# Kernel tuning notes

Hardware: AMD Instinct MI355X
Metric: run time of the kernel (lower is better)

Reference implementation:

```python
import math
import jax, jax.numpy as jnp
import numpy as np

EPS = 1e-5
RATIO = 0.5


def gcn_conv(x, src, dst, ew, W, b):
    # GCNConv(add_self_loops=True, normalize=True, improved=True): self-loop fill = 2.0
    N = x.shape[0]
    h = x @ W  # [N, Cout]
    deg = jax.ops.segment_sum(ew, dst, num_segments=N) + 2.0
    dinv = jnp.where(deg > 0, deg ** -0.5, 0.0)
    norm = dinv[src] * ew * dinv[dst]  # [E]
    agg = jax.ops.segment_sum(h[src] * norm[:, None], dst, num_segments=N)
    return agg + (2.0 * dinv * dinv)[:, None] * h + b


def batch_norm(x, g, b):
    # training-mode BatchNorm1d over nodes (biased variance)
    mu = x.mean(0)
    var = x.var(0)
    return (x - mu) * jax.lax.rsqrt(var + EPS) * g + b


def topk_pool(x, src, dst, ew, p):
    # TopKPooling: score = tanh(x.p/||p||), keep top ceil(ratio*N), x' = x[perm]*score[perm]
    N = x.shape[0]
    k = int(math.ceil(RATIO * N))
    score = jnp.tanh((x @ p) / jnp.linalg.norm(p))
    vals, perm = jax.lax.top_k(score, k)
    xk = x[perm] * vals[:, None]
    new_idx = jnp.full((N,), -1, jnp.int32).at[perm].set(jnp.arange(k, dtype=jnp.int32))
    ns, nd = new_idx[src], new_idx[dst]
    keep = (ns >= 0) & (nd >= 0)
    # keep fixed edge count; dropped edges get weight 0 -> contribute nothing
    return xk, jnp.where(keep, ns, 0), jnp.where(keep, nd, 0), jnp.where(keep, ew, 0.0), perm


def encode(x, src, dst, ew, mW, mb, g1, b1, cW, cb, g2, b2):
    x = batch_norm(jax.nn.relu(x @ mW + mb), g1, b1)  # MLP: Lin -> ReLU -> BN
    x = gcn_conv(x, src, dst, ew, cW, cb)
    return jax.nn.relu(batch_norm(x, g2, b2))


def unet(x, edge_src, edge_dst,
         e0_mlp_W, e0_mlp_b, e0_bn1_g, e0_bn1_b, e0_conv_W, e0_conv_b, e0_n_g, e0_n_b,
         e1_p, e1_mlp_W, e1_mlp_b, e1_bn1_g, e1_bn1_b, e1_conv_W, e1_conv_b, e1_n_g, e1_n_b,
         e2_p, e2_mlp_W, e2_mlp_b, e2_bn1_g, e2_bn1_b, e2_conv_W, e2_conv_b, e2_n_g, e2_n_b,
         d2_W, d2_b, d1_W, d1_b, d0_W, d0_b):
    E = edge_src.shape[0]
    ew0 = jnp.ones((E,), x.dtype)
    # encoder0 (no pool)
    x1 = encode(x, edge_src, edge_dst, ew0, e0_mlp_W, e0_mlp_b, e0_bn1_g, e0_bn1_b,
                e0_conv_W, e0_conv_b, e0_n_g, e0_n_b)
    # encoder1 (pool 0.5)
    xp, s1, t1, ew1, perm1 = topk_pool(x1, edge_src, edge_dst, ew0, e1_p)
    x2 = encode(xp, s1, t1, ew1, e1_mlp_W, e1_mlp_b, e1_bn1_g, e1_bn1_b,
                e1_conv_W, e1_conv_b, e1_n_g, e1_n_b)
    # encoder2 (pool 0.5)
    xp, s2, t2, ew2, perm2 = topk_pool(x2, s1, t1, ew1, e2_p)
    x3 = encode(xp, s2, t2, ew2, e2_mlp_W, e2_mlp_b, e2_bn1_g, e2_bn1_b,
                e2_conv_W, e2_conv_b, e2_n_g, e2_n_b)
    # decoder2 + unpool into x2 via perm2: up[perm]=(x+res[perm])/2, up[~perm]=res
    d = jax.nn.relu(gcn_conv(x3, s2, t2, ew2, d2_W, d2_b))
    xu = x2.at[perm2].set((d + x2[perm2]) * 0.5)
    # decoder1 + unpool into x1 via perm1
    d = jax.nn.relu(gcn_conv(xu, s1, t1, ew1, d1_W, d1_b))
    xu = x1.at[perm1].set((d + x1[perm1]) * 0.5)
    # decoder0 on the original graph, no activation
    return gcn_conv(xu, edge_src, edge_dst, ew0, d0_W, d0_b)


def setup_inputs() -> dict:
    key = jax.random.key(0)
    N, E, C = 100000, 1600000, [16, 64, 128, 256]
    ks = iter(jax.random.split(key, 64))
    nk = lambda: next(ks)

    def glorot(shape):
        s = math.sqrt(6.0 / (shape[0] + shape[1]))
        return jax.random.uniform(nk(), shape, minval=-s, maxval=s, dtype=jnp.float32)

    inp = {
        'x': jax.random.normal(nk(), (N, C[0]), jnp.float32),
        'edge_src': jax.random.randint(nk(), (E,), 0, N, jnp.int32),
        'edge_dst': jax.random.randint(nk(), (E,), 0, N, jnp.int32),
    }
    for i, (ci, co) in enumerate(zip(C[:-1], C[1:])):
        pre = f'e{i}_'
        if i > 0:
            inp[pre + 'p'] = jax.random.normal(nk(), (ci,), jnp.float32)
        inp[pre + 'mlp_W'] = glorot((ci, co)); inp[pre + 'mlp_b'] = jnp.zeros((co,), jnp.float32)
        inp[pre + 'bn1_g'] = jnp.ones((co,), jnp.float32); inp[pre + 'bn1_b'] = jnp.zeros((co,), jnp.float32)
        inp[pre + 'conv_W'] = glorot((co, co)); inp[pre + 'conv_b'] = jnp.zeros((co,), jnp.float32)
        inp[pre + 'n_g'] = jnp.ones((co,), jnp.float32); inp[pre + 'n_b'] = jnp.zeros((co,), jnp.float32)
    inp['d2_W'] = glorot((256, 128)); inp['d2_b'] = jnp.zeros((128,), jnp.float32)
    inp['d1_W'] = glorot((128, 64)); inp['d1_b'] = jnp.zeros((64,), jnp.float32)
    inp['d0_W'] = glorot((64, 16)); inp['d0_b'] = jnp.zeros((16,), jnp.float32)
    return inp


def reference(x, edge_src, edge_dst,
              e0_mlp_W, e0_mlp_b, e0_bn1_g, e0_bn1_b, e0_conv_W, e0_conv_b, e0_n_g, e0_n_b,
              e1_p, e1_mlp_W, e1_mlp_b, e1_bn1_g, e1_bn1_b, e1_conv_W, e1_conv_b, e1_n_g, e1_n_b,
              e2_p, e2_mlp_W, e2_mlp_b, e2_bn1_g, e2_bn1_b, e2_conv_W, e2_conv_b, e2_n_g, e2_n_b,
              d2_W, d2_b, d1_W, d1_b, d0_W, d0_b):
    return unet(x, edge_src, edge_dst,
                e0_mlp_W, e0_mlp_b, e0_bn1_g, e0_bn1_b, e0_conv_W, e0_conv_b, e0_n_g, e0_n_b,
                e1_p, e1_mlp_W, e1_mlp_b, e1_bn1_g, e1_bn1_b, e1_conv_W, e1_conv_b, e1_n_g, e1_n_b,
                e2_p, e2_mlp_W, e2_mlp_b, e2_bn1_g, e2_bn1_b, e2_conv_W, e2_conv_b, e2_n_g, e2_n_b,
                d2_W, d2_b, d1_W, d1_b, d0_W, d0_b)
```

## Files before the change

### kernel.cpp

```cpp
#include <hip/hip_runtime.h>
#include <math.h>

static inline int cdiv(int a, int b){ return (a + b - 1) / b; }

#define SCAN_CHUNK 4096
#define BCHUNK 4096

typedef _Float16 v4h __attribute__((ext_vector_type(4)));
typedef float    v4f __attribute__((ext_vector_type(4)));
typedef _Float16 h2  __attribute__((ext_vector_type(2)));


__global__ void k_count0(const int* __restrict__ dst, int* __restrict__ cnt, int E){
  int i = blockIdx.x*blockDim.x + threadIdx.x;
  if (i < E) atomicAdd(&cnt[dst[i]], 1);
}

__global__ __launch_bounds__(256) void k_bucket(const int* __restrict__ src, const int* __restrict__ dst,
                        int E, int* __restrict__ gcur, unsigned int* __restrict__ bout){
  __shared__ int lcnt[256], gbase[256];
  int t = threadIdx.x;
  lcnt[t] = 0;
  __syncthreads();
  int base = blockIdx.x*BCHUNK;
  int end = min(base + BCHUNK, E);
  for (int i = base + t; i < end; i += 256) atomicAdd(&lcnt[dst[i] >> 9], 1);
  __syncthreads();
  gbase[t] = lcnt[t] ? atomicAdd(&gcur[t], lcnt[t]) : 0;
  __syncthreads();
  lcnt[t] = 0;
  __syncthreads();
  for (int i = base + t; i < end; i += 256){
    int s = src[i], d = dst[i];
    int b = d >> 9;
    int pos = gbase[b] + atomicAdd(&lcnt[b], 1);
    bout[pos] = ((unsigned int)s << 9) | (unsigned int)(d & 511);
  }
}

__global__ __launch_bounds__(256) void k_fill_b(const unsigned int* __restrict__ bout,
                        const int* __restrict__ rowptr, int* __restrict__ fillg,
                        int* __restrict__ cols, int N, int BPB){
  int b = blockIdx.x / BPB, sub = blockIdx.x % BPB;
  int r0 = b << 9;
  int r1 = min(r0 + 512, N);
  int start = rowptr[r0], end = rowptr[r1];
  for (int i = start + sub*256 + threadIdx.x; i < end; i += BPB*256){
    unsigned int v = bout[i];
    int d = r0 + (int)(v & 511u);
    int pos = rowptr[d] + atomicAdd(&fillg[d], 1);
    cols[pos] = (int)(v >> 9);
  }
}


__global__ __launch_bounds__(256) void k_csr_keep(const int* __restrict__ rowptrA, const int* __restrict__ colsA,
                         const int* __restrict__ nidx, int* __restrict__ tmp,
                         int* __restrict__ cnt, int NA){
  int t = threadIdx.x;
  int g = (blockIdx.x*256 + t) >> 4;
  int lane = t & 15;
  if (g >= NA) return;
  int m = nidx[g];
  if (m < 0) return;
  int jb = rowptrA[g], je = rowptrA[g+1];
  int run = 0;
  int shift = (t & 63) & ~15;
  for (int j0 = jb; j0 < je; j0 += 16){
    int j = j0 + lane;
    int s = -1;
    if (j < je) s = nidx[colsA[j]];
    bool keep = s >= 0;
    unsigned long long bal = __ballot(keep);
    unsigned int gm = (unsigned int)(bal >> shift) & 0xFFFFu;
    if (keep) tmp[jb + run + __popc(gm & ((1u << lane) - 1))] = s;
    run += __popc(gm);
  }
  if (lane == 0) cnt[m] = run;
}

__global__ __launch_bounds__(256) void k_csr_copy(const int* __restrict__ rowptrA, const int* __restrict__ nidx,
                         const int* __restrict__ tmp, const int* __restrict__ rowptrB,
                         int* __restrict__ colsB, int NA){
  int t = threadIdx.x;
  int g = (blockIdx.x*256 + t) >> 4;
  int lane = t & 15;
  if (g >= NA) return;
  int m = nidx[g];
  if (m < 0) return;
  int jbA = rowptrA[g];
  int db = rowptrB[m], n = rowptrB[m+1] - db;
  for (int j = lane; j < n; j += 16) colsB[db + j] = tmp[jbA + j];
}


__global__ __launch_bounds__(256) void k_scan_p1(const int* __restrict__ in, int nIn, int* __restrict__ bsum){
  __shared__ int sh[256];
  int base = blockIdx.x*SCAN_CHUNK;
  int end = min(base + SCAN_CHUNK, nIn);
  int s = 0;
  for (int i = base + threadIdx.x; i < end; i += 256) s += in[i];
  sh[threadIdx.x] = s; __syncthreads();
  for (int o = 128; o > 0; o >>= 1){
    if (threadIdx.x < o) sh[threadIdx.x] += sh[threadIdx.x + o];
    __syncthreads();
  }
  if (threadIdx.x == 0) bsum[blockIdx.x] = sh[0];
}

__global__ __launch_bounds__(256) void k_scan_p2(int* __restrict__ bsum, int nb){
  __shared__ int sh[256];
  int t = threadIdx.x;
  int v = (t < nb) ? bsum[t] : 0;
  sh[t] = v; __syncthreads();
  for (int o = 1; o < 256; o <<= 1){
    int u = (t >= o) ? sh[t-o] : 0;
    __syncthreads();
    sh[t] += u;
    __syncthreads();
  }
  if (t < nb) bsum[t] = sh[t] - v;
}

__global__ __launch_bounds__(256) void k_scan_p3(const int* __restrict__ cnt, const int* __restrict__ bsum,
                        int* __restrict__ rowptr, float* __restrict__ dinv,
                        int* __restrict__ gcur, int nIn){
  int t = threadIdx.x;
  int tb = blockIdx.x*SCAN_CHUNK + t*16;
  int my[16]; int s = 0;
#pragma unroll
  for (int j = 0; j < 16; ++j){
    int i = tb + j;
    int v = (i < nIn) ? cnt[i] : 0;
    my[j] = v; s += v;
  }
  __shared__ int sh[256];
  sh[t] = s; __syncthreads();
  for (int o = 1; o < 256; o <<= 1){
    int u = (t >= o) ? sh[t-o] : 0;
    __syncthreads();
    sh[t] += u;
    __syncthreads();
  }
  int run = bsum[blockIdx.x] + sh[t] - s;
#pragma unroll
  for (int j = 0; j < 16; ++j){
    int i = tb + j;
    if (i < nIn){
      rowptr[i] = run;
      if (dinv) dinv[i] = rsqrtf((float)my[j] + 2.0f);
      if (gcur && (i & 511) == 0) gcur[i >> 9] = run;
      run += my[j];
    } else if (i == nIn){
      rowptr[nIn] = run;
    }
  }
}


__global__ void k_prep_w_el(const float* __restrict__ W, const float* __restrict__ ss,
                            _Float16* __restrict__ Whi, _Float16* __restrict__ Wlo,
                            float* __restrict__ bias2, const float* __restrict__ bias,
                            int KM, int M, int mshift, int mmask){
  int idx = blockIdx.x*256 + threadIdx.x;
  if (idx >= KM) return;
  int k = idx >> mshift, m = idx & mmask;
  float w = W[idx];
  if (ss) w *= ss[k];
  _Float16 hi = (_Float16)w;
  size_t oidx = ((size_t)(k >> 2)*M + m)*4 + (k & 3);
  Whi[oidx] = hi;
  if (Wlo) Wlo[oidx] = (_Float16)(w - (float)hi);
  if (k == 0) bias2[m] = bias ? bias[m] : 0.f;
}

__global__ void k_prep_bias(const float* __restrict__ W, const float* __restrict__ ss,
                            float* __restrict__ bias2, int K, int M){
  int m = blockIdx.x;
  int lane = threadIdx.x;
  float s = 0.f;
  for (int k = lane; k < K; k += 64) s = fmaf(ss[K + k], W[(size_t)k*M + m], s);
  for (int o = 32; o > 0; o >>= 1) s += __shfl_down(s, o, 64);
  if (lane == 0) bias2[m] = s;
}


template<int SPLIT>
__global__ __launch_bounds__(256) void k_gemm16(
    const float* __restrict__ A, const _Float16* __restrict__ Whi,
    const _Float16* __restrict__ Wlo, const float* __restrict__ bias2,
    float* __restrict__ Out32, _Float16* __restrict__ Out16,
    float* __restrict__ stats, const int* __restrict__ permA,
    const float* __restrict__ valA, int N, int K, int M, int relu)
{
  __shared__ float sacc[64], s2acc[64];
  int tid = threadIdx.x;
  if (stats){
    if (tid < 64){ sacc[tid] = 0.f; s2acc[tid] = 0.f; }
    __syncthreads();
  }
  int wave = tid >> 6, lane = tid & 63;
  int g = lane >> 4, r = lane & 15;
  int wrow0 = blockIdx.x*256 + wave*64;
  int col0 = blockIdx.y*64;
  int nf = (M - col0) >> 4; if (nf > 4) nf = 4;

  int srow[4]; float sclr[4];
#pragma unroll
  for (int rt = 0; rt < 4; ++rt){
    int arow = wrow0 + rt*16 + r;
    if (arow < N){
      int sr = permA ? permA[arow] : arow;
      srow[rt] = sr;
      sclr[rt] = permA ? valA[sr] : 1.f;
    } else { srow[rt] = -1; sclr[rt] = 0.f; }
  }

  v4f acc[4][4];
#pragma unroll
  for (int rt = 0; rt < 4; ++rt)
#pragma unroll
    for (int c = 0; c < 4; ++c) acc[rt][c] = (v4f){0.f,0.f,0.f,0.f};

  for (int k0 = 0; k0 < K; k0 += 16){
    int kb = (k0 >> 2) + g;
    v4h bh[4], bl[4];
#pragma unroll
    for (int c = 0; c < 4; ++c){
      if (c >= nf) continue;
      size_t bidx = ((size_t)kb*M + col0 + c*16 + r)*4;
      bh[c] = *(const v4h*)&Whi[bidx];
      if (SPLIT) bl[c] = *(const v4h*)&Wlo[bidx];
    }
    v4h ah[4], al[4];
#pragma unroll
    for (int rt = 0; rt < 4; ++rt){
      if (srow[rt] >= 0){
        float4 av = *(const float4*)&A[(size_t)srow[rt]*K + k0 + g*4];
        float xs[4] = {av.x*sclr[rt], av.y*sclr[rt], av.z*sclr[rt], av.w*sclr[rt]};
#pragma unroll
        for (int j = 0; j < 4; ++j){
          _Float16 hi = (_Float16)xs[j];
          ah[rt][j] = hi;
          if (SPLIT) al[rt][j] = (_Float16)(xs[j] - (float)hi);
        }
      } else {
#pragma unroll
        for (int j = 0; j < 4; ++j){ ah[rt][j] = (_Float16)0.f; if (SPLIT) al[rt][j] = (_Float16)0.f; }
      }
    }
#pragma unroll
    for (int rt = 0; rt < 4; ++rt){
#pragma unroll
      for (int c = 0; c < 4; ++c){
        if (c >= nf) continue;
        acc[rt][c] = __builtin_amdgcn_mfma_f32_16x16x16f16(ah[rt], bh[c], acc[rt][c], 0, 0, 0);
        if (SPLIT){
          acc[rt][c] = __builtin_amdgcn_mfma_f32_16x16x16f16(al[rt], bh[c], acc[rt][c], 0, 0, 0);
          acc[rt][c] = __builtin_amdgcn_mfma_f32_16x16x16f16(ah[rt], bl[c], acc[rt][c], 0, 0, 0);
        }
      }
    }
  }

#pragma unroll
  for (int c = 0; c < 4; ++c){
    if (c >= nf) continue;
    int col = col0 + c*16 + r;
    float bsv = bias2[col];
    float s = 0.f, s2 = 0.f;
#pragma unroll
    for (int rt = 0; rt < 4; ++rt){
#pragma unroll
      for (int i = 0; i < 4; ++i){
        int rr = wrow0 + rt*16 + g*4 + i;
        float v = acc[rt][c][i] + bsv;
        if (relu) v = fmaxf(v, 0.f);
        if (rr < N){
          if (Out32) Out32[(size_t)rr*M + col] = v;
          if (Out16) Out16[(size_t)rr*M + col] = (_Float16)v;
          s += v; s2 = fmaf(v, v, s2);
        }
      }
    }
    if (stats){
      s  += __shfl_xor(s, 16);  s  += __shfl_xor(s, 32);
      s2 += __shfl_xor(s2, 16); s2 += __shfl_xor(s2, 32);
      if (g == 0){
        atomicAdd(&sacc[c*16 + r], s);
        atomicAdd(&s2acc[c*16 + r], s2);
      }
    }
  }
  if (stats){
    __syncthreads();
    if (tid < 64 && col0 + tid < M){
      atomicAdd(&stats[col0 + tid], sacc[tid]);
      atomicAdd(&stats[M + col0 + tid], s2acc[tid]);
    }
  }
}


__global__ void k_bn_stats(const float* __restrict__ X, float* __restrict__ acc, int N, int C){
  int col = threadIdx.x % C;
  int rg  = threadIdx.x / C;
  int R   = blockDim.x / C;
  float s = 0.f, s2 = 0.f;
  for (int r = blockIdx.x*R + rg; r < N; r += gridDim.x*R){
    float v = X[(size_t)r*C + col];
    s += v; s2 += v*v;
  }
  __shared__ float sh[256], sh2[256];
  sh[threadIdx.x] = s; sh2[threadIdx.x] = s2;
  __syncthreads();
  if (rg == 0){
    for (int r = 1; r < R; ++r){ s += sh[r*C + col]; s2 += sh2[r*C + col]; }
    atomicAdd(&acc[col], s);
    atomicAdd(&acc[C + col], s2);
  }
}

__global__ void k_bn_final(const float* __restrict__ acc, const float* __restrict__ g,
                           const float* __restrict__ b, float* __restrict__ ss, int N, int C){
  int c = threadIdx.x;
  if (c >= C) return;
  float mu  = acc[c] / (float)N;
  float var = acc[C + c] / (float)N - mu*mu;
  float sc  = rsqrtf(var + 1e-5f) * g[c];
  ss[c]     = sc;
  ss[C + c] = b[c] - mu*sc;
}

__global__ void k_bn_apply(const float* __restrict__ X, float* __restrict__ Y,
                           const float* __restrict__ ss, int total, int C, int relu){
  int i = blockIdx.x*blockDim.x + threadIdx.x;
  if (i >= total) return;
  int c = i % C;
  float v = X[i]*ss[c] + ss[C + c];
  if (relu) v = fmaxf(v, 0.f);
  Y[i] = v;
}

__global__ void k_bnap_score(const float* __restrict__ X, float* __restrict__ Y,
                             const float* __restrict__ ss, const float* __restrict__ p,
                             float* __restrict__ val, unsigned int* __restrict__ key,
                             int N, int C){
  int wid  = (blockIdx.x*blockDim.x + threadIdx.x) >> 6;
  int lane = threadIdx.x & 63;
  if (wid >= N) return;
  float s = 0.f, np = 0.f;
  for (int c = lane; c < C; c += 64){
    float v = X[(size_t)wid*C + c]*ss[c] + ss[C + c];
    v = fmaxf(v, 0.f);
    Y[(size_t)wid*C + c] = v;
    float pv = p[c];
    s = fmaf(v, pv, s);
    np = fmaf(pv, pv, np);
  }
  for (int o = 32; o > 0; o >>= 1){ s += __shfl_down(s, o, 64); np += __shfl_down(np, o, 64); }
  if (lane == 0){
    float sc = tanhf(s * rsqrtf(np));
    val[wid] = sc;
    unsigned int b = __float_as_uint(sc);
    key[wid] = (b & 0x80000000u) ? ~b : (b | 0x80000000u);
  }
}


__device__ inline float2 ldpair(const float* h, size_t off){
  return *(const float2*)(h + off);
}
__device__ inline float2 ldpair(const _Float16* h, size_t off){
  h2 v = *(const h2*)(h + off);
  return make_float2((float)v[0], (float)v[1]);
}

template<int C, typename T>
__global__ void k_agg(const T* __restrict__ h, const int* __restrict__ rowptr,
                      const int* __restrict__ cols, const float* __restrict__ dinv,
                      const float* __restrict__ bias, float* __restrict__ out,
                      int N, int relu)
{
  constexpr int PAIRS = C/2;
  constexpr int TPN = (PAIRS < 64) ? PAIRS : 64;
  constexpr int R = PAIRS / TPN;
  int gid  = blockIdx.x*blockDim.x + threadIdx.x;
  int node = gid / TPN;
  int lane = gid % TPN;
  if (node >= N) return;
  float di = dinv[node];
  float2 acc[R];
#pragma unroll
  for (int r = 0; r < R; ++r) acc[r] = make_float2(0.f, 0.f);
  int j  = rowptr[node];
  int je = rowptr[node+1];
  for (; j + 4 <= je; j += 4){
    int s0 = cols[j], s1 = cols[j+1], s2 = cols[j+2], s3 = cols[j+3];
    float w0 = dinv[s0]*di, w1 = dinv[s1]*di, w2 = dinv[s2]*di, w3 = dinv[s3]*di;
#pragma unroll
    for (int r = 0; r < R; ++r){
      size_t po = (size_t)(lane + r*TPN)*2;
      float2 h0 = ldpair(h, (size_t)s0*C + po);
      float2 h1 = ldpair(h, (size_t)s1*C + po);
      float2 h2v = ldpair(h, (size_t)s2*C + po);
      float2 h3 = ldpair(h, (size_t)s3*C + po);
      acc[r].x = fmaf(w0, h0.x, acc[r].x); acc[r].y = fmaf(w0, h0.y, acc[r].y);
      acc[r].x = fmaf(w1, h1.x, acc[r].x); acc[r].y = fmaf(w1, h1.y, acc[r].y);
      acc[r].x = fmaf(w2, h2v.x, acc[r].x); acc[r].y = fmaf(w2, h2v.y, acc[r].y);
      acc[r].x = fmaf(w3, h3.x, acc[r].x); acc[r].y = fmaf(w3, h3.y, acc[r].y);
    }
  }
  for (; j < je; ++j){
    int s = cols[j];
    float wgt = dinv[s]*di;
#pragma unroll
    for (int r = 0; r < R; ++r){
      float2 hv = ldpair(h, (size_t)s*C + (size_t)(lane + r*TPN)*2);
      acc[r].x = fmaf(wgt, hv.x, acc[r].x);
      acc[r].y = fmaf(wgt, hv.y, acc[r].y);
    }
  }
  float sw = 2.f*di*di;
#pragma unroll
  for (int r = 0; r < R; ++r){
    int pc = (lane + r*TPN)*2;
    float2 hv = ldpair(h, (size_t)node*C + pc);
    float2 v;
    v.x = acc[r].x + sw*hv.x + bias[pc];
    v.y = acc[r].y + sw*hv.y + bias[pc+1];
    if (relu){ v.x = fmaxf(v.x, 0.f); v.y = fmaxf(v.y, 0.f); }
    *(float2*)&out[(size_t)node*C + pc] = v;
  }
}

template<typename T>
static void launch_agg(const T* h, const int* rp, const int* cl, const float* dv,
                       const float* bias, float* o, int N, int C, int relu, hipStream_t stream){
  int tpn = (C/2 < 64) ? C/2 : 64;
  dim3 g(cdiv(N*tpn, 256));
  switch (C){
    case 16:  k_agg<16,T> <<<g, dim3(256), 0, stream>>>(h, rp, cl, dv, bias, o, N, relu); break;
    case 64:  k_agg<64,T> <<<g, dim3(256), 0, stream>>>(h, rp, cl, dv, bias, o, N, relu); break;
    case 128: k_agg<128,T><<<g, dim3(256), 0, stream>>>(h, rp, cl, dv, bias, o, N, relu); break;
    case 256: k_agg<256,T><<<g, dim3(256), 0, stream>>>(h, rp, cl, dv, bias, o, N, relu); break;
  }
}


__global__ void k_hist_hi(const unsigned int* __restrict__ key, int N, unsigned int* __restrict__ hist){
  int i = blockIdx.x*blockDim.x + threadIdx.x;
  if (i < N) atomicAdd(&hist[key[i] >> 16], 1u);
}

__global__ void k_hist_lo(const unsigned int* __restrict__ key, int N,
                          const int* __restrict__ state, unsigned int* __restrict__ hist){
  int i = blockIdx.x*blockDim.x + threadIdx.x;
  if (i >= N) return;
  unsigned int kk = key[i];
  if ((int)(kk >> 16) == state[1]) atomicAdd(&hist[kk & 0xffffu], 1u);
}

__global__ void k_scan_hist(unsigned int* __restrict__ hist, int* __restrict__ state,
                            int karg, int kidx, int bidx, int ridx){
  __shared__ unsigned int part[1024];
  __shared__ unsigned int suff[1024];
  int t = threadIdx.x;
  unsigned int s = 0;
  int base = t*64;
  for (int j = 0; j < 64; ++j) s += hist[base + j];
  part[t] = s;
  suff[t] = s;
  __syncthreads();
  for (int o = 1; o < 1024; o <<= 1){
    unsigned int v = (t + o < 1024) ? suff[t + o] : 0u;
    __syncthreads();
    suff[t] += v;
    __syncthreads();
  }
  unsigned int k = (unsigned int)((kidx >= 0) ? state[kidx] : karg);
  unsigned int above = suff[t] - part[t];
  if (above < k && above + part[t] >= k){
    unsigned int cum = above;
    for (int b = 63; b >= 0; --b){
      unsigned int c = hist[base + b];
      if (cum + c >= k){ state[bidx] = base + b; state[ridx] = (int)(k - cum); break; }
      cum += c;
    }
  }
  __syncthreads();
  for (int j = 0; j < 64; ++j) hist[base + j] = 0u;
}

__global__ __launch_bounds__(256) void k_sel_p1(const unsigned int* __restrict__ key, int n,
                       const int* __restrict__ state, int2* __restrict__ bcnt){
  unsigned int T = ((unsigned int)state[1] << 16) | (unsigned int)state[3];
  int base = blockIdx.x*SCAN_CHUNK;
  int end = min(base + SCAN_CHUNK, n);
  int gt = 0, eq = 0;
  for (int i = base + threadIdx.x; i < end; i += 256){
    unsigned int v = key[i];
    gt += (v > T); eq += (v == T);
  }
  __shared__ int sg[256], se[256];
  sg[threadIdx.x] = gt; se[threadIdx.x] = eq;
  __syncthreads();
  for (int o = 128; o > 0; o >>= 1){
    if (threadIdx.x < o){ sg[threadIdx.x] += sg[threadIdx.x + o]; se[threadIdx.x] += se[threadIdx.x + o]; }
    __syncthreads();
  }
  if (threadIdx.x == 0) bcnt[blockIdx.x] = make_int2(sg[0], se[0]);
}

__global__ __launch_bounds__(256) void k_sel_p2(int2* __restrict__ bcnt, int nb){
  __shared__ int sg[256], se[256];
  int t = threadIdx.x;
  int2 v = (t < nb) ? bcnt[t] : make_int2(0, 0);
  sg[t] = v.x; se[t] = v.y; __syncthreads();
  for (int o = 1; o < 256; o <<= 1){
    int a = (t >= o) ? sg[t-o] : 0;
    int b = (t >= o) ? se[t-o] : 0;
    __syncthreads();
    sg[t] += a; se[t] += b;
    __syncthreads();
  }
  if (t < nb) bcnt[t] = make_int2(sg[t] - v.x, se[t] - v.y);
}

__global__ __launch_bounds__(256) void k_sel_p3(const unsigned int* __restrict__ key, int n,
                       const int* __restrict__ state, const int2* __restrict__ bcnt,
                       int* __restrict__ nidx, int* __restrict__ perm){
  unsigned int T = ((unsigned int)state[1] << 16) | (unsigned int)state[3];
  int m = state[4];
  int t = threadIdx.x;
  int tb = blockIdx.x*SCAN_CHUNK + t*16;
  unsigned int kk[16];
  int gt = 0, eq = 0;
#pragma unroll
  for (int j = 0; j < 16; ++j){
    int i = tb + j;
    bool ok = i < n;
    unsigned int v = ok ? key[i] : 0u;
    kk[j] = v;
    gt += (ok && v > T); eq += (ok && v == T);
  }
  __shared__ unsigned long long sh[256];
  unsigned long long mine = ((unsigned long long)(unsigned)gt << 32) | (unsigned)eq;
  sh[t] = mine; __syncthreads();
  for (int o = 1; o < 256; o <<= 1){
    unsigned long long u = (t >= o) ? sh[t-o] : 0ull;
    __syncthreads();
    sh[t] += u;
    __syncthreads();
  }
  unsigned long long excl = sh[t] - mine;
  int2 bo = bcnt[blockIdx.x];
  int gb = bo.x + (int)(excl >> 32);
  int eb = bo.y + (int)(excl & 0xffffffffu);
#pragma unroll
  for (int j = 0; j < 16; ++j){
    int i = tb + j;
    if (i >= n) break;
    unsigned int v = kk[j];
    bool g = v > T, e = v == T;
    bool sel = g || (e && eb < m);
    if (sel){
      int ni = gb + (eb < m ? eb : m);
      nidx[i] = ni;
      perm[ni] = i;
    } else nidx[i] = -1;
    gb += g; eb += e;
  }
}

__global__ void k_unpool(float* __restrict__ X, const float* __restrict__ D,
                         const int* __restrict__ nidx, int N, int C){
  int i = blockIdx.x*blockDim.x + threadIdx.x;
  int n = i / C, c = i % C;
  if (n >= N) return;
  int m = nidx[n];
  if (m >= 0) X[i] = (D[(size_t)m*C + c] + X[i])*0.5f;
}


extern "C" void kernel_launch(void* const* d_in, const int* in_sizes, int n_in,
                              void* d_out, int out_size, void* d_ws, size_t ws_size,
                              hipStream_t stream)
{
  const float* x_in = (const float*)d_in[0];
  const int*   esrc = (const int*)d_in[1];
  const int*   edst = (const int*)d_in[2];
  const float* e0_mlp_W = (const float*)d_in[3];
  const float* e0_mlp_b = (const float*)d_in[4];
  const float* e0_bn1_g = (const float*)d_in[5];
  const float* e0_bn1_b = (const float*)d_in[6];
  const float* e0_conv_W= (const float*)d_in[7];
  const float* e0_conv_b= (const float*)d_in[8];
  const float* e0_n_g   = (const float*)d_in[9];
  const float* e0_n_b   = (const float*)d_in[10];
  const float* e1_p     = (const float*)d_in[11];
  const float* e1_mlp_W = (const float*)d_in[12];
  const float* e1_mlp_b = (const float*)d_in[13];
  const float* e1_bn1_g = (const float*)d_in[14];
  const float* e1_bn1_b = (const float*)d_in[15];
  const float* e1_conv_W= (const float*)d_in[16];
  const float* e1_conv_b= (const float*)d_in[17];
  const float* e1_n_g   = (const float*)d_in[18];
  const float* e1_n_b   = (const float*)d_in[19];
  const float* e2_p     = (const float*)d_in[20];
  const float* e2_mlp_W = (const float*)d_in[21];
  const float* e2_mlp_b = (const float*)d_in[22];
  const float* e2_bn1_g = (const float*)d_in[23];
  const float* e2_bn1_b = (const float*)d_in[24];
  const float* e2_conv_W= (const float*)d_in[25];
  const float* e2_conv_b= (const float*)d_in[26];
  const float* e2_n_g   = (const float*)d_in[27];
  const float* e2_n_b   = (const float*)d_in[28];
  const float* d2_W = (const float*)d_in[29];
  const float* d2_b = (const float*)d_in[30];
  const float* d1_W = (const float*)d_in[31];
  const float* d1_b = (const float*)d_in[32];
  const float* d0_W = (const float*)d_in[33];
  const float* d0_b = (const float*)d_in[34];
  float* out = (float*)d_out;

  const int N0 = in_sizes[0] / 16;
  const int E  = in_sizes[1];
  const int N1 = (N0 + 1) / 2;
  const int N2 = (N1 + 1) / 2;
  const int NB0 = cdiv(N0, 512);

  char* w = (char*)d_ws;
  auto alloc = [&](size_t b)->void*{ void* p = (void*)w; w += (b + 255) & ~(size_t)255; return p; };
  float* x1 = (float*)alloc((size_t)N0*64*4);
  float* x2 = (float*)alloc((size_t)N1*128*4);
  float* x3 = (float*)alloc((size_t)N2*256*4);
  size_t tmax = (size_t)N0*64*4;
  float* tA = (float*)alloc(tmax);
  float* tB = (float*)alloc(tmax);
  _Float16* h16 = (_Float16*)alloc((size_t)N0*64*2);
  int* rowptr0 = (int*)alloc((size_t)(N0+1)*4);
  int* rowptr1 = (int*)alloc((size_t)(N1+1)*4);
  int* rowptr2 = (int*)alloc((size_t)(N2+1)*4);
  int* cnt  = (int*)alloc((size_t)(N0+1)*4);
  int* fillg = (int*)alloc((size_t)N0*4);
  int* cols0 = (int*)alloc((size_t)E*4);
  int* cols1 = (int*)alloc((size_t)E*4);
  int* cols2 = (int*)alloc((size_t)E*4);
  float* dinv0 = (float*)alloc((size_t)N0*4);
  float* dinv1 = (float*)alloc((size_t)N1*4);
  float* dinv2 = (float*)alloc((size_t)N2*4);
  int* nidx1 = (int*)alloc((size_t)N0*4);
  int* nidx2 = (int*)alloc((size_t)N1*4);
  int* perm1 = (int*)alloc((size_t)N1*4);
  int* perm2 = (int*)alloc((size_t)N2*4);
  float* val = (float*)alloc((size_t)N0*4);
  unsigned int* key = (unsigned int*)alloc((size_t)N0*4);
  unsigned int* hist = (unsigned int*)alloc((size_t)65536*4);
  int* state = (int*)alloc(64);
  int* bsum = (int*)alloc(1024*4);
  int2* bcnt = (int2*)alloc(1024*8);
  int* gcur = (int*)alloc(256*4);
  float* bnacc = (float*)alloc(512*4);
  float* ss = (float*)alloc(512*4);
  _Float16* whi = (_Float16*)alloc((size_t)256*256*2);
  _Float16* wlo = (_Float16*)alloc((size_t)256*256*2);
  float* bias2 = (float*)alloc(256*4);
  if ((size_t)(w - (char*)d_ws) > ws_size) return;
  unsigned int* bout = (unsigned int*)tA;
  int* tmpE = (int*)tA;

  auto run_prep = [&](const float* W, const float* bias, int K, int M, int split){
    int KM = K*M;
    k_prep_w_el<<<dim3(cdiv(KM,256)), dim3(256), 0, stream>>>(
        W, nullptr, whi, split ? wlo : nullptr, bias2, bias, KM, M, __builtin_ctz(M), M-1);
  };
  auto run_prep_bn = [&](const float* W, const float* g, const float* b, int Ncount, int K, int M, int split){
    k_bn_final<<<dim3(1), dim3(K), 0, stream>>>(bnacc, g, b, ss, Ncount, K);
    int KM = K*M;
    k_prep_w_el<<<dim3(cdiv(KM,256)), dim3(256), 0, stream>>>(
        W, ss, whi, split ? wlo : nullptr, bias2, nullptr, KM, M, __builtin_ctz(M), M-1);
    k_prep_bias<<<dim3(M), dim3(64), 0, stream>>>(W, ss, bias2, K, M);
  };
  auto run_gemm = [&](const float* A, float* O32, _Float16* O16, float* stats,
                      const int* perm, int N, int K, int M, int act, int split){
    dim3 grd(cdiv(N,256), cdiv(M,64));
    if (split)
      k_gemm16<1><<<grd, dim3(256), 0, stream>>>(A, whi, wlo, bias2, O32, O16, stats, perm, val, N, K, M, act);
    else
      k_gemm16<0><<<grd, dim3(256), 0, stream>>>(A, whi, wlo, bias2, O32, O16, stats, perm, val, N, K, M, act);
  };
  auto run_scan = [&](const int* in, int* rowptr, float* dinv, int* gc, int nIn){
    int nb = cdiv(nIn + 1, SCAN_CHUNK);
    k_scan_p1<<<dim3(nb), dim3(256), 0, stream>>>(in, nIn, bsum);
    k_scan_p2<<<dim3(1), dim3(256), 0, stream>>>(bsum, nb);
    k_scan_p3<<<dim3(nb), dim3(256), 0, stream>>>(in, bsum, rowptr, dinv, gc, nIn);
  };
  auto run_topk_rest = [&](int N, int k, int* nidx, int* perm){
    k_hist_hi<<<dim3(cdiv(N,256)), dim3(256), 0, stream>>>(key, N, hist);
    k_scan_hist<<<dim3(1), dim3(1024), 0, stream>>>(hist, state, k, -1, 1, 2);
    k_hist_lo<<<dim3(cdiv(N,256)), dim3(256), 0, stream>>>(key, N, state, hist);
    k_scan_hist<<<dim3(1), dim3(1024), 0, stream>>>(hist, state, 0, 2, 3, 4);
    int nb = cdiv(N, SCAN_CHUNK);
    k_sel_p1<<<dim3(nb), dim3(256), 0, stream>>>(key, N, state, bcnt);
    k_sel_p2<<<dim3(1), dim3(256), 0, stream>>>(bcnt, nb);
    k_sel_p3<<<dim3(nb), dim3(256), 0, stream>>>(key, N, state, bcnt, nidx, perm);
  };
  auto run_csr_derive = [&](const int* rpA, const int* clA, const int* nidx,
                            int* rpB, int* clB, float* dvB, int NA, int NB){
    k_csr_keep<<<dim3(cdiv(NA*16,256)), dim3(256), 0, stream>>>(rpA, clA, nidx, tmpE, cnt, NA);
    run_scan(cnt, rpB, dvB, nullptr, NB);
    k_csr_copy<<<dim3(cdiv(NA*16,256)), dim3(256), 0, stream>>>(rpA, nidx, tmpE, rpB, clB, NA);
  };

  hipMemsetAsync(hist, 0, 65536*4, stream);

  hipMemsetAsync(cnt, 0, (size_t)(N0+1)*4, stream);
  k_count0<<<dim3(cdiv(E,256)), dim3(256), 0, stream>>>(edst, cnt, E);
  run_scan(cnt, rowptr0, dinv0, gcur, N0);
  k_bucket<<<dim3(cdiv(E,BCHUNK)), dim3(256), 0, stream>>>(esrc, edst, E, gcur, bout);
  hipMemsetAsync(fillg, 0, (size_t)N0*4, stream);
  k_fill_b<<<dim3(NB0*4), dim3(256), 0, stream>>>(bout, rowptr0, fillg, cols0, N0, 4);

  hipMemsetAsync(bnacc, 0, 2*64*4, stream);
  run_prep(e0_mlp_W, e0_mlp_b, 16, 64, 1);
  run_gemm(x_in, tA, nullptr, bnacc, nullptr, N0, 16, 64, 1, 1);
  run_prep_bn(e0_conv_W, e0_bn1_g, e0_bn1_b, N0, 64, 64, 1);
  run_gemm(tA, tB, nullptr, nullptr, nullptr, N0, 64, 64, 0, 1);
  launch_agg<float>(tB, rowptr0, cols0, dinv0, e0_conv_b, tA, N0, 64, 0, stream);
  hipMemsetAsync(bnacc, 0, 2*64*4, stream);
  k_bn_stats<<<dim3(256), dim3(256), 0, stream>>>(tA, bnacc, N0, 64);
  k_bn_final<<<dim3(1), dim3(64), 0, stream>>>(bnacc, e0_n_g, e0_n_b, ss, N0, 64);
  k_bnap_score<<<dim3(cdiv(N0*64,256)), dim3(256), 0, stream>>>(tA, x1, ss, e1_p, val, key, N0, 64);

  run_topk_rest(N0, N1, nidx1, perm1);
  run_csr_derive(rowptr0, cols0, nidx1, rowptr1, cols1, dinv1, N0, N1);

  hipMemsetAsync(bnacc, 0, 2*128*4, stream);
  run_prep(e1_mlp_W, e1_mlp_b, 64, 128, 1);
  run_gemm(x1, tB, nullptr, bnacc, perm1, N1, 64, 128, 1, 1);
  run_prep_bn(e1_conv_W, e1_bn1_g, e1_bn1_b, N1, 128, 128, 1);
  run_gemm(tB, tA, nullptr, nullptr, nullptr, N1, 128, 128, 0, 1);
  launch_agg<float>(tA, rowptr1, cols1, dinv1, e1_conv_b, tB, N1, 128, 0, stream);
  hipMemsetAsync(bnacc, 0, 2*128*4, stream);
  k_bn_stats<<<dim3(256), dim3(256), 0, stream>>>(tB, bnacc, N1, 128);
  k_bn_final<<<dim3(1), dim3(128), 0, stream>>>(bnacc, e1_n_g, e1_n_b, ss, N1, 128);
  k_bnap_score<<<dim3(cdiv(N1*64,256)), dim3(256), 0, stream>>>(tB, x2, ss, e2_p, val, key, N1, 128);

  run_topk_rest(N1, N2, nidx2, perm2);
  run_csr_derive(rowptr1, cols1, nidx2, rowptr2, cols2, dinv2, N1, N2);

  hipMemsetAsync(bnacc, 0, 2*256*4, stream);
  run_prep(e2_mlp_W, e2_mlp_b, 128, 256, 0);
  run_gemm(x2, tB, nullptr, bnacc, perm2, N2, 128, 256, 1, 0);
  run_prep_bn(e2_conv_W, e2_bn1_g, e2_bn1_b, N2, 256, 256, 0);
  run_gemm(tB, nullptr, h16, nullptr, nullptr, N2, 256, 256, 0, 0);
  launch_agg<_Float16>(h16, rowptr2, cols2, dinv2, e2_conv_b, tB, N2, 256, 0, stream);
  hipMemsetAsync(bnacc, 0, 2*256*4, stream);
  k_bn_stats<<<dim3(256), dim3(256), 0, stream>>>(tB, bnacc, N2, 256);
  k_bn_final<<<dim3(1), dim3(256), 0, stream>>>(bnacc, e2_n_g, e2_n_b, ss, N2, 256);
  k_bn_apply<<<dim3(cdiv(N2*256,256)), dim3(256), 0, stream>>>(tB, x3, ss, N2*256, 256, 1);

  run_prep(d2_W, nullptr, 256, 128, 0);
  run_gemm(x3, nullptr, h16, nullptr, nullptr, N2, 256, 128, 0, 0);
  launch_agg<_Float16>(h16, rowptr2, cols2, dinv2, d2_b, tB, N2, 128, 1, stream);
  k_unpool<<<dim3(cdiv(N1*128,256)), dim3(256), 0, stream>>>(x2, tB, nidx2, N1, 128);

  run_prep(d1_W, nullptr, 128, 64, 0);
  run_gemm(x2, nullptr, h16, nullptr, nullptr, N1, 128, 64, 0, 0);
  launch_agg<_Float16>(h16, rowptr1, cols1, dinv1, d1_b, tB, N1, 64, 1, stream);
  k_unpool<<<dim3(cdiv(N0*64,256)), dim3(256), 0, stream>>>(x1, tB, nidx1, N0, 64);

  run_prep(d0_W, nullptr, 64, 16, 0);
  run_gemm(x1, nullptr, h16, nullptr, nullptr, N0, 64, 16, 0, 0);
  launch_agg<_Float16>(h16, rowptr0, cols0, dinv0, d0_b, out, N0, 16, 0, stream);
}
```

Baseline: 1.194 ms.

## Fuse BN stats into aggregation, rebuild CSR per bucket, parallelize top-k histogram scan

BatchNorm statistics are now accumulated inside the aggregation kernel through shared-memory atomics, which removes the separate full read of the aggregated output. CSR construction replaces the per-node global count, scan and fill with a bucket-level count and scan. A per-bucket kernel then computes rowptr, dinv and column placement using shared-memory counters. The single-block 1024-thread histogram scan for top-k becomes a two-level parallel reduce-and-pick, with memsets for clearing. In exchange it adds many shared float atomics in aggregation and extra histogram memsets per top-k.

Result: slower. 1.660 ms (+39.1%).

```diff
diff --git a/kernel.cpp b/kernel.cpp
--- a/kernel.cpp
+++ b/kernel.cpp
@@ -11,9 +11,31 @@
 typedef _Float16 h2  __attribute__((ext_vector_type(2)));
 
 
-__global__ void k_count0(const int* __restrict__ dst, int* __restrict__ cnt, int E){
-  int i = blockIdx.x*blockDim.x + threadIdx.x;
-  if (i < E) atomicAdd(&cnt[dst[i]], 1);
+__global__ __launch_bounds__(256) void k_bcount(const int* __restrict__ dst, int E, int* __restrict__ bcnt256){
+  __shared__ int h[256];
+  h[threadIdx.x] = 0;
+  __syncthreads();
+  int stride = gridDim.x*256;
+  for (int i = blockIdx.x*256 + threadIdx.x; i < E; i += stride) atomicAdd(&h[dst[i] >> 9], 1);
+  __syncthreads();
+  if (h[threadIdx.x]) atomicAdd(&bcnt256[threadIdx.x], h[threadIdx.x]);
+}
+
+__global__ __launch_bounds__(256) void k_scan_b256(const int* __restrict__ bcnt256, int* __restrict__ bbase,
+                          int* __restrict__ gcur, int NB){
+  __shared__ int sh[256];
+  int t = threadIdx.x;
+  int v = (t < NB) ? bcnt256[t] : 0;
+  sh[t] = v; __syncthreads();
+  for (int o = 1; o < 256; o <<= 1){
+    int u = (t >= o) ? sh[t-o] : 0;
+    __syncthreads();
+    sh[t] += u;
+    __syncthreads();
+  }
+  int excl = sh[t] - v;
+  if (t < NB){ bbase[t] = excl; gcur[t] = excl; }
+  if (t == 0) bbase[NB] = sh[255];
 }
 
 __global__ __launch_bounds__(256) void k_bucket(const int* __restrict__ src, const int* __restrict__ dst,
@@ -38,17 +60,39 @@
   }
 }
 
-__global__ __launch_bounds__(256) void k_fill_b(const unsigned int* __restrict__ bout,
-                        const int* __restrict__ rowptr, int* __restrict__ fillg,
-                        int* __restrict__ cols, int N, int BPB){
-  int b = blockIdx.x / BPB, sub = blockIdx.x % BPB;
+__global__ __launch_bounds__(256) void k_build(const unsigned int* __restrict__ bout, const int* __restrict__ bbase,
+                       int* __restrict__ rowptr, float* __restrict__ dinv,
+                       int* __restrict__ cols, int N, int NB){
+  __shared__ int cnt[512], part[256];
+  int b = blockIdx.x;
+  int t = threadIdx.x;
+  cnt[t] = 0; cnt[t + 256] = 0;
+  __syncthreads();
+  int s0 = bbase[b], s1 = bbase[b+1];
+  for (int i = s0 + t; i < s1; i += 256) atomicAdd(&cnt[bout[i] & 511u], 1);
+  __syncthreads();
+  int c0 = cnt[2*t], c1 = cnt[2*t + 1];
+  part[t] = c0 + c1;
+  __syncthreads();
+  for (int o = 1; o < 256; o <<= 1){
+    int u = (t >= o) ? part[t-o] : 0;
+    __syncthreads();
+    part[t] += u;
+    __syncthreads();
+  }
+  int e0 = part[t] - (c0 + c1);
+  int e1 = e0 + c0;
   int r0 = b << 9;
-  int r1 = min(r0 + 512, N);
-  int start = rowptr[r0], end = rowptr[r1];
-  for (int i = start + sub*256 + threadIdx.x; i < end; i += BPB*256){
+  int n0 = r0 + 2*t, n1 = n0 + 1;
+  if (n0 < N){ rowptr[n0] = s0 + e0; dinv[n0] = rsqrtf((float)c0 + 2.f); }
+  if (n1 < N){ rowptr[n1] = s0 + e1; dinv[n1] = rsqrtf((float)c1 + 2.f); }
+  if (b == NB-1 && t == 0) rowptr[N] = s1;
+  __syncthreads();
+  cnt[2*t] = s0 + e0; cnt[2*t + 1] = s0 + e1;
+  __syncthreads();
+  for (int i = s0 + t; i < s1; i += 256){
     unsigned int v = bout[i];
-    int d = r0 + (int)(v & 511u);
-    int pos = rowptr[d] + atomicAdd(&fillg[d], 1);
+    int pos = atomicAdd(&cnt[v & 511u], 1);
     cols[pos] = (int)(v >> 9);
   }
 }
@@ -123,8 +167,7 @@
 }
 
 __global__ __launch_bounds__(256) void k_scan_p3(const int* __restrict__ cnt, const int* __restrict__ bsum,
-                        int* __restrict__ rowptr, float* __restrict__ dinv,
-                        int* __restrict__ gcur, int nIn){
+                        int* __restrict__ rowptr, float* __restrict__ dinv, int nIn){
   int t = threadIdx.x;
   int tb = blockIdx.x*SCAN_CHUNK + t*16;
   int my[16]; int s = 0;
@@ -149,7 +192,6 @@
     if (i < nIn){
       rowptr[i] = run;
       if (dinv) dinv[i] = rsqrtf((float)my[j] + 2.0f);
-      if (gcur && (i & 511) == 0) gcur[i >> 9] = run;
       run += my[j];
     } else if (i == nIn){
       rowptr[nIn] = run;
@@ -301,25 +343,6 @@
   }
 }
 
-
-__global__ void k_bn_stats(const float* __restrict__ X, float* __restrict__ acc, int N, int C){
-  int col = threadIdx.x % C;
-  int rg  = threadIdx.x / C;
-  int R   = blockDim.x / C;
-  float s = 0.f, s2 = 0.f;
-  for (int r = blockIdx.x*R + rg; r < N; r += gridDim.x*R){
-    float v = X[(size_t)r*C + col];
-    s += v; s2 += v*v;
-  }
-  __shared__ float sh[256], sh2[256];
-  sh[threadIdx.x] = s; sh2[threadIdx.x] = s2;
-  __syncthreads();
-  if (rg == 0){
-    for (int r = 1; r < R; ++r){ s += sh[r*C + col]; s2 += sh2[r*C + col]; }
-    atomicAdd(&acc[col], s);
-    atomicAdd(&acc[C + col], s2);
-  }
-}
 
 __global__ void k_bn_final(const float* __restrict__ acc, const float* __restrict__ g,
                            const float* __restrict__ b, float* __restrict__ ss, int N, int C){
@@ -380,70 +403,98 @@
 __global__ void k_agg(const T* __restrict__ h, const int* __restrict__ rowptr,
                       const int* __restrict__ cols, const float* __restrict__ dinv,
                       const float* __restrict__ bias, float* __restrict__ out,
-                      int N, int relu)
+                      float* __restrict__ stats, int N, int relu)
 {
   constexpr int PAIRS = C/2;
   constexpr int TPN = (PAIRS < 64) ? PAIRS : 64;
   constexpr int R = PAIRS / TPN;
-  int gid  = blockIdx.x*blockDim.x + threadIdx.x;
+  __shared__ float ls[256], ls2[256];
+  int t = threadIdx.x;
+  if (stats){
+    ls[t] = 0.f; ls2[t] = 0.f;
+    __syncthreads();
+  }
+  int gid  = blockIdx.x*blockDim.x + t;
   int node = gid / TPN;
   int lane = gid % TPN;
-  if (node >= N) return;
-  float di = dinv[node];
-  float2 acc[R];
-#pragma unroll
-  for (int r = 0; r < R; ++r) acc[r] = make_float2(0.f, 0.f);
-  int j  = rowptr[node];
-  int je = rowptr[node+1];
-  for (; j + 4 <= je; j += 4){
-    int s0 = cols[j], s1 = cols[j+1], s2 = cols[j+2], s3 = cols[j+3];
-    float w0 = dinv[s0]*di, w1 = dinv[s1]*di, w2 = dinv[s2]*di, w3 = dinv[s3]*di;
+  bool act = node < N;
+  float2 vv[R];
+  if (act){
+    float di = dinv[node];
+    float2 acc[R];
+#pragma unroll
+    for (int r = 0; r < R; ++r) acc[r] = make_float2(0.f, 0.f);
+    int j  = rowptr[node];
+    int je = rowptr[node+1];
+    for (; j + 4 <= je; j += 4){
+      int s0 = cols[j], s1 = cols[j+1], s2 = cols[j+2], s3 = cols[j+3];
+      float w0 = dinv[s0]*di, w1 = dinv[s1]*di, w2 = dinv[s2]*di, w3 = dinv[s3]*di;
+#pragma unroll
+      for (int r = 0; r < R; ++r){
+        size_t po = (size_t)(lane + r*TPN)*2;
+        float2 h0 = ldpair(h, (size_t)s0*C + po);
+        float2 h1 = ldpair(h, (size_t)s1*C + po);
+        float2 h2v = ldpair(h, (size_t)s2*C + po);
+        float2 h3 = ldpair(h, (size_t)s3*C + po);
+        acc[r].x = fmaf(w0, h0.x, acc[r].x); acc[r].y = fmaf(w0, h0.y, acc[r].y);
+        acc[r].x = fmaf(w1, h1.x, acc[r].x); acc[r].y = fmaf(w1, h1.y, acc[r].y);
+        acc[r].x = fmaf(w2, h2v.x, acc[r].x); acc[r].y = fmaf(w2, h2v.y, acc[r].y);
+        acc[r].x = fmaf(w3, h3.x, acc[r].x); acc[r].y = fmaf(w3, h3.y, acc[r].y);
+      }
+    }
+    for (; j < je; ++j){
+      int s = cols[j];
+      float wgt = dinv[s]*di;
+#pragma unroll
+      for (int r = 0; r < R; ++r){
+        float2 hv = ldpair(h, (size_t)s*C + (size_t)(lane + r*TPN)*2);
+        acc[r].x = fmaf(wgt, hv.x, acc[r].x);
+        acc[r].y = fmaf(wgt, hv.y, acc[r].y);
+      }
+    }
+    float sw = 2.f*di*di;
 #pragma unroll
     for (int r = 0; r < R; ++r){
-      size_t po = (size_t)(lane + r*TPN)*2;
-      float2 h0 = ldpair(h, (size_t)s0*C + po);
-      float2 h1 = ldpair(h, (size_t)s1*C + po);
-      float2 h2v = ldpair(h, (size_t)s2*C + po);
-      float2 h3 = ldpair(h, (size_t)s3*C + po);
-      acc[r].x = fmaf(w0, h0.x, acc[r].x); acc[r].y = fmaf(w0, h0.y, acc[r].y);
-      acc[r].x = fmaf(w1, h1.x, acc[r].x); acc[r].y = fmaf(w1, h1.y, acc[r].y);
-      acc[r].x = fmaf(w2, h2v.x, acc[r].x); acc[r].y = fmaf(w2, h2v.y, acc[r].y);
-      acc[r].x = fmaf(w3, h3.x, acc[r].x); acc[r].y = fmaf(w3, h3.y, acc[r].y);
-    }
-  }
-  for (; j < je; ++j){
-    int s = cols[j];
-    float wgt = dinv[s]*di;
-#pragma unroll
-    for (int r = 0; r < R; ++r){
-      float2 hv = ldpair(h, (size_t)s*C + (size_t)(lane + r*TPN)*2);
-      acc[r].x = fmaf(wgt, hv.x, acc[r].x);
-      acc[r].y = fmaf(wgt, hv.y, acc[r].y);
-    }
-  }
-  float sw = 2.f*di*di;
-#pragma unroll
-  for (int r = 0; r < R; ++r){
-    int pc = (lane + r*TPN)*2;
-    float2 hv = ldpair(h, (size_t)node*C + pc);
-    float2 v;
-    v.x = acc[r].x + sw*hv.x + bias[pc];
-    v.y = acc[r].y + sw*hv.y + bias[pc+1];
-    if (relu){ v.x = fmaxf(v.x, 0.f); v.y = fmaxf(v.y, 0.f); }
-    *(float2*)&out[(size_t)node*C + pc] = v;
+      int pc = (lane + r*TPN)*2;
+      float2 hv = ldpair(h, (size_t)node*C + pc);
+      float2 v;
+      v.x = acc[r].x + sw*hv.x + bias[pc];
+      v.y = acc[r].y + sw*hv.y + bias[pc+1];
+      if (relu){ v.x = fmaxf(v.x, 0.f); v.y = fmaxf(v.y, 0.f); }
+      *(float2*)&out[(size_t)node*C + pc] = v;
+      vv[r] = v;
+    }
+  }
+  if (stats){
+    if (act){
+#pragma unroll
+      for (int r = 0; r < R; ++r){
+        int pc = (lane + r*TPN)*2;
+        atomicAdd(&ls[pc], vv[r].x);
+        atomicAdd(&ls[pc+1], vv[r].y);
+        atomicAdd(&ls2[pc], vv[r].x*vv[r].x);
+        atomicAdd(&ls2[pc+1], vv[r].y*vv[r].y);
+      }
+    }
+    __syncthreads();
+    if (t < C){
+      atomicAdd(&stats[t], ls[t]);
+      atomicAdd(&stats[C + t], ls2[t]);
+    }
   }
 }
 
 template<typename T>
 static void launch_agg(const T* h, const int* rp, const int* cl, const float* dv,
-                       const float* bias, float* o, int N, int C, int relu, hipStream_t stream){
+                       const float* bias, float* o, float* stats, int N, int C, int relu,
+                       hipStream_t stream){
   int tpn = (C/2 < 64) ? C/2 : 64;
   dim3 g(cdiv(N*tpn, 256));
   switch (C){
-    case 16:  k_agg<16,T> <<<g, dim3(256), 0, stream>>>(h, rp, cl, dv, bias, o, N, relu); break;
-    case 64:  k_agg<64,T> <<<g, dim3(256), 0, stream>>>(h, rp, cl, dv, bias, o, N, relu); break;
-    case 128: k_agg<128,T><<<g, dim3(256), 0, stream>>>(h, rp, cl, dv, bias, o, N, relu); break;
-    case 256: k_agg<256,T><<<g, dim3(256), 0, stream>>>(h, rp, cl, dv, bias, o, N, relu); break;
+    case 16:  k_agg<16,T> <<<g, dim3(256), 0, stream>>>(h, rp, cl, dv, bias, o, stats, N, relu); break;
+    case 64:  k_agg<64,T> <<<g, dim3(256), 0, stream>>>(h, rp, cl, dv, bias, o, stats, N, relu); break;
+    case 128: k_agg<128,T><<<g, dim3(256), 0, stream>>>(h, rp, cl, dv, bias, o, stats, N, relu); break;
+    case 256: k_agg<256,T><<<g, dim3(256), 0, stream>>>(h, rp, cl, dv, bias, o, stats, N, relu); break;
   }
 }
 
@@ -461,35 +512,46 @@
   if ((int)(kk >> 16) == state[1]) atomicAdd(&hist[kk & 0xffffu], 1u);
 }
 
-__global__ void k_scan_hist(unsigned int* __restrict__ hist, int* __restrict__ state,
-                            int karg, int kidx, int bidx, int ridx){
-  __shared__ unsigned int part[1024];
-  __shared__ unsigned int suff[1024];
-  int t = threadIdx.x;
-  unsigned int s = 0;
-  int base = t*64;
-  for (int j = 0; j < 64; ++j) s += hist[base + j];
-  part[t] = s;
-  suff[t] = s;
-  __syncthreads();
-  for (int o = 1; o < 1024; o <<= 1){
-    unsigned int v = (t + o < 1024) ? suff[t + o] : 0u;
-    __syncthreads();
-    suff[t] += v;
+__global__ __launch_bounds__(256) void k_hsum(const unsigned int* __restrict__ hist, unsigned int* __restrict__ hsum){
+  __shared__ unsigned int sh[256];
+  unsigned int v = hist[blockIdx.x*256 + threadIdx.x];
+  sh[threadIdx.x] = v; __syncthreads();
+  for (int o = 128; o > 0; o >>= 1){
+    if (threadIdx.x < o) sh[threadIdx.x] += sh[threadIdx.x + o];
+    __syncthreads();
+  }
+  if (threadIdx.x == 0) hsum[blockIdx.x] = sh[0];
+}
+
+__global__ __launch_bounds__(256) void k_hpick(const unsigned int* __restrict__ hist, const unsigned int* __restrict__ hsum,
+                       int* __restrict__ state, int karg, int kidx, int bidx, int ridx){
+  __shared__ unsigned int sh[256];
+  __shared__ int Bsel;
+  __shared__ unsigned int aboveB;
+  int t = threadIdx.x;
+  unsigned int v = hsum[t];
+  sh[t] = v; __syncthreads();
+  for (int o = 1; o < 256; o <<= 1){
+    unsigned int u = (t + o < 256) ? sh[t + o] : 0u;
+    __syncthreads();
+    sh[t] += u;
     __syncthreads();
   }
   unsigned int k = (unsigned int)((kidx >= 0) ? state[kidx] : karg);
-  unsigned int above = suff[t] - part[t];
-  if (above < k && above + part[t] >= k){
-    unsigned int cum = above;
-    for (int b = 63; b >= 0; --b){
-      unsigned int c = hist[base + b];
-      if (cum + c >= k){ state[bidx] = base + b; state[ridx] = (int)(k - cum); break; }
-      cum += c;
-    }
-  }
-  __syncthreads();
-  for (int j = 0; j < 64; ++j) hist[base + j] = 0u;
+  unsigned int above = sh[t] - v;
+  if (above < k && sh[t] >= k){ Bsel = t; aboveB = above; }
+  __syncthreads();
+  int B = Bsel; unsigned int ab = aboveB;
+  unsigned int c = hist[B*256 + t];
+  sh[t] = c; __syncthreads();
+  for (int o = 1; o < 256; o <<= 1){
+    unsigned int u = (t + o < 256) ? sh[t + o] : 0u;
+    __syncthreads();
+    sh[t] += u;
+    __syncthreads();
+  }
+  unsigned int above2 = ab + sh[t] - c;
+  if (above2 < k && above2 + c >= k){ state[bidx] = B*256 + t; state[ridx] = (int)(k - above2); }
 }
 
 __global__ __launch_bounds__(256) void k_sel_p1(const unsigned int* __restrict__ key, int n,
@@ -643,7 +705,6 @@
   int* rowptr1 = (int*)alloc((size_t)(N1+1)*4);
   int* rowptr2 = (int*)alloc((size_t)(N2+1)*4);
   int* cnt  = (int*)alloc((size_t)(N0+1)*4);
-  int* fillg = (int*)alloc((size_t)N0*4);
   int* cols0 = (int*)alloc((size_t)E*4);
   int* cols1 = (int*)alloc((size_t)E*4);
   int* cols2 = (int*)alloc((size_t)E*4);
@@ -657,10 +718,13 @@
   float* val = (float*)alloc((size_t)N0*4);
   unsigned int* key = (unsigned int*)alloc((size_t)N0*4);
   unsigned int* hist = (unsigned int*)alloc((size_t)65536*4);
+  unsigned int* hsum = (unsigned int*)alloc(256*4);
   int* state = (int*)alloc(64);
   int* bsum = (int*)alloc(1024*4);
   int2* bcnt = (int2*)alloc(1024*8);
   int* gcur = (int*)alloc(256*4);
+  int* bcnt256 = (int*)alloc(256*4);
+  int* bbase = (int*)alloc(257*4);
   float* bnacc = (float*)alloc(512*4);
   float* ss = (float*)alloc(512*4);
   _Float16* whi = (_Float16*)alloc((size_t)256*256*2);
@@ -690,17 +754,21 @@
     else
       k_gemm16<0><<<grd, dim3(256), 0, stream>>>(A, whi, wlo, bias2, O32, O16, stats, perm, val, N, K, M, act);
   };
-  auto run_scan = [&](const int* in, int* rowptr, float* dinv, int* gc, int nIn){
+  auto run_scan = [&](const int* in, int* rowptr, float* dinv, int nIn){
     int nb = cdiv(nIn + 1, SCAN_CHUNK);
     k_scan_p1<<<dim3(nb), dim3(256), 0, stream>>>(in, nIn, bsum);
     k_scan_p2<<<dim3(1), dim3(256), 0, stream>>>(bsum, nb);
-    k_scan_p3<<<dim3(nb), dim3(256), 0, stream>>>(in, bsum, rowptr, dinv, gc, nIn);
+    k_scan_p3<<<dim3(nb), dim3(256), 0, stream>>>(in, bsum, rowptr, dinv, nIn);
   };
   auto run_topk_rest = [&](int N, int k, int* nidx, int* perm){
+    hipMemsetAsync(hist, 0, 65536*4, stream);
     k_hist_hi<<<dim3(cdiv(N,256)), dim3(256), 0, stream>>>(key, N, hist);
-    k_scan_hist<<<dim3(1), dim3(1024), 0, stream>>>(hist, state, k, -1, 1, 2);
+    k_hsum<<<dim3(256), dim3(256), 0, stream>>>(hist, hsum);
+    k_hpick<<<dim3(1), dim3(256), 0, stream>>>(hist, hsum, state, k, -1, 1, 2);
+    hipMemsetAsync(hist, 0, 65536*4, stream);
     k_hist_lo<<<dim3(cdiv(N,256)), dim3(256), 0, stream>>>(key, N, state, hist);
-    k_scan_hist<<<dim3(1), dim3(1024), 0, stream>>>(hist, state, 0, 2, 3, 4);
+    k_hsum<<<dim3(256), dim3(256), 0, stream>>>(hist, hsum);
+    k_hpick<<<dim3(1), dim3(256), 0, stream>>>(hist, hsum, state, 0, 2, 3, 4);
     int nb = cdiv(N, SCAN_CHUNK);
     k_sel_p1<<<dim3(nb), dim3(256), 0, stream>>>(key, N, state, bcnt);
     k_sel_p2<<<dim3(1), dim3(256), 0, stream>>>(bcnt, nb);
@@ -709,27 +777,23 @@
   auto run_csr_derive = [&](const int* rpA, const int* clA, const int* nidx,
                             int* rpB, int* clB, float* dvB, int NA, int NB){
     k_csr_keep<<<dim3(cdiv(NA*16,256)), dim3(256), 0, stream>>>(rpA, clA, nidx, tmpE, cnt, NA);
-    run_scan(cnt, rpB, dvB, nullptr, NB);
+    run_scan(cnt, rpB, dvB, NB);
     k_csr_copy<<<dim3(cdiv(NA*16,256)), dim3(256), 0, stream>>>(rpA, nidx, tmpE, rpB, clB, NA);
   };
 
-  hipMemsetAsync(hist, 0, 65536*4, stream);
-
-  hipMemsetAsync(cnt, 0, (size_t)(N0+1)*4, stream);
-  k_count0<<<dim3(cdiv(E,256)), dim3(256), 0, stream>>>(edst, cnt, E);
-  run_scan(cnt, rowptr0, dinv0, gcur, N0);
+  hipMemsetAsync(bcnt256, 0, 256*4, stream);
+  k_bcount<<<dim3(64), dim3(256), 0, stream>>>(edst, E, bcnt256);
+  k_scan_b256<<<dim3(1), dim3(256), 0, stream>>>(bcnt256, bbase, gcur, NB0);
   k_bucket<<<dim3(cdiv(E,BCHUNK)), dim3(256), 0, stream>>>(esrc, edst, E, gcur, bout);
-  hipMemsetAsync(fillg, 0, (size_t)N0*4, stream);
-  k_fill_b<<<dim3(NB0*4), dim3(256), 0, stream>>>(bout, rowptr0, fillg, cols0, N0, 4);
+  k_build<<<dim3(NB0), dim3(256), 0, stream>>>(bout, bbase, rowptr0, dinv0, cols0, N0, NB0);
 
   hipMemsetAsync(bnacc, 0, 2*64*4, stream);
   run_prep(e0_mlp_W, e0_mlp_b, 16, 64, 1);
   run_gemm(x_in, tA, nullptr, bnacc, nullptr, N0, 16, 64, 1, 1);
   run_prep_bn(e0_conv_W, e0_bn1_g, e0_bn1_b, N0, 64, 64, 1);
   run_gemm(tA, tB, nullptr, nullptr, nullptr, N0, 64, 64, 0, 1);
-  launch_agg<float>(tB, rowptr0, cols0, dinv0, e0_conv_b, tA, N0, 64, 0, stream);
   hipMemsetAsync(bnacc, 0, 2*64*4, stream);
-  k_bn_stats<<<dim3(256), dim3(256), 0, stream>>>(tA, bnacc, N0, 64);
+  launch_agg<float>(tB, rowptr0, cols0, dinv0, e0_conv_b, tA, bnacc, N0, 64, 0, stream);
   k_bn_final<<<dim3(1), dim3(64), 0, stream>>>(bnacc, e0_n_g, e0_n_b, ss, N0, 64);
   k_bnap_score<<<dim3(cdiv(N0*64,256)), dim3(256), 0, stream>>>(tA, x1, ss, e1_p, val, key, N0, 64);
 
@@ -741,9 +805,8 @@
   run_gemm(x1, tB, nullptr, bnacc, perm1, N1, 64, 128, 1, 1);
   run_prep_bn(e1_conv_W, e1_bn1_g, e1_bn1_b, N1, 128, 128, 1);
   run_gemm(tB, tA, nullptr, nullptr, nullptr, N1, 128, 128, 0, 1);
-  launch_agg<float>(tA, rowptr1, cols1, dinv1, e1_conv_b, tB, N1, 128, 0, stream);
   hipMemsetAsync(bnacc, 0, 2*128*4, stream);
-  k_bn_stats<<<dim3(256), dim3(256), 0, stream>>>(tB, bnacc, N1, 128);
+  launch_agg<float>(tA, rowptr1, cols1, dinv1, e1_conv_b, tB, bnacc, N1, 128, 0, stream);
   k_bn_final<<<dim3(1), dim3(128), 0, stream>>>(bnacc, e1_n_g, e1_n_b, ss, N1, 128);
   k_bnap_score<<<dim3(cdiv(N1*64,256)), dim3(256), 0, stream>>>(tB, x2, ss, e2_p, val, key, N1, 128);
 
@@ -755,23 +818,22 @@
   run_gemm(x2, tB, nullptr, bnacc, perm2, N2, 128, 256, 1, 0);
   run_prep_bn(e2_conv_W, e2_bn1_g, e2_bn1_b, N2, 256, 256, 0);
   run_gemm(tB, nullptr, h16, nullptr, nullptr, N2, 256, 256, 0, 0);
-  launch_agg<_Float16>(h16, rowptr2, cols2, dinv2, e2_conv_b, tB, N2, 256, 0, stream);
   hipMemsetAsync(bnacc, 0, 2*256*4, stream);
-  k_bn_stats<<<dim3(256), dim3(256), 0, stream>>>(tB, bnacc, N2, 256);
+  launch_agg<_Float16>(h16, rowptr2, cols2, dinv2, e2_conv_b, tB, bnacc, N2, 256, 0, stream);
   k_bn_final<<<dim3(1), dim3(256), 0, stream>>>(bnacc, e2_n_g, e2_n_b, ss, N2, 256);
   k_bn_apply<<<dim3(cdiv(N2*256,256)), dim3(256), 0, stream>>>(tB, x3, ss, N2*256, 256, 1);
 
   run_prep(d2_W, nullptr, 256, 128, 0);
   run_gemm(x3, nullptr, h16, nullptr, nullptr, N2, 256, 128, 0, 0);
-  launch_agg<_Float16>(h16, rowptr2, cols2, dinv2, d2_b, tB, N2, 128, 1, stream);
+  launch_agg<_Float16>(h16, rowptr2, cols2, dinv2, d2_b, tB, nullptr, N2, 128, 1, stream);
   k_unpool<<<dim3(cdiv(N1*128,256)), dim3(256), 0, stream>>>(x2, tB, nidx2, N1, 128);
 
   run_prep(d1_W, nullptr, 128, 64, 0);
   run_gemm(x2, nullptr, h16, nullptr, nullptr, N1, 128, 64, 0, 0);
-  launch_agg<_Float16>(h16, rowptr1, cols1, dinv1, d1_b, tB, N1, 64, 1, stream);
+  launch_agg<_Float16>(h16, rowptr1, cols1, dinv1, d1_b, tB, nullptr, N1, 64, 1, stream);
   k_unpool<<<dim3(cdiv(N0*64,256)), dim3(256), 0, stream>>>(x1, tB, nidx1, N0, 64);
 
   run_prep(d0_W, nullptr, 64, 16, 0);
   run_gemm(x1, nullptr, h16, nullptr, nullptr, N0, 64, 16, 0, 0);
-  launch_agg<_Float16>(h16, rowptr0, cols0, dinv0, d0_b, out, N0, 16, 0, stream);
-}
+  launch_agg<_Float16>(h16, rowptr0, cols0, dinv0, d0_b, out, nullptr, N0, 16, 0, stream);
+}
```
